# Optimization experiments

Hardware: AMD Instinct MI355X
Metric: run time of the kernel (lower is better)

Reference implementation:

```python
import jax, jax.numpy as jnp
import numpy as np

N_NODES = 100000
N_EDGES = 1600000
IN_DIM = 128
OUT_DIM = 128
NEG_SLOPE = 0.2


def setup_inputs() -> dict:
    key = jax.random.key(0)
    ks = jax.random.split(key, 7)
    x = jax.random.normal(ks[0], (N_NODES, IN_DIM), dtype=jnp.float32)
    edge_index = jax.random.randint(ks[1], (2, N_EDGES), 0, N_NODES, dtype=jnp.int32)
    # xavier-ish scale for [in, out] weight layout (y = x @ W)
    s = float(np.sqrt(2.0 / (IN_DIM + OUT_DIM)))
    W_q = jax.random.normal(ks[2], (IN_DIM, OUT_DIM), dtype=jnp.float32) * s
    W_k = jax.random.normal(ks[3], (IN_DIM, OUT_DIM), dtype=jnp.float32) * s
    W_v = jax.random.normal(ks[4], (IN_DIM, OUT_DIM), dtype=jnp.float32) * s
    W_l = jax.random.normal(ks[5], (IN_DIM, OUT_DIM), dtype=jnp.float32) * s
    b_l = jnp.zeros((OUT_DIM,), dtype=jnp.float32)
    return {"x": x, "edge_index": edge_index, "W_q": W_q, "W_k": W_k,
            "W_v": W_v, "W_l": W_l, "b_l": b_l}


def reference(x, edge_index, W_q, W_k, W_v, W_l, b_l):
    num_nodes = x.shape[0]
    row, col = edge_index[0], edge_index[1]

    h_q = x @ W_q                                   # [N, D]
    h_k = x @ W_k                                   # [N, D]
    _h_v = x @ W_v                                  # computed in original, unused downstream

    # aggregated query: sum of neighbor queries per destination node
    q_agg = jax.ops.segment_sum(h_q[col], row, num_segments=num_nodes)  # [N, D]
    k_act = jax.nn.leaky_relu(h_k, NEG_SLOPE)

    # per-edge attention scores (note: original uses raw q_agg, not activated)
    scores = jnp.sum(k_act[row] * q_agg[col], axis=1) / (OUT_DIM ** 0.5)  # [E]

    # scatter-softmax over edges grouped by destination (row)
    max_val = jax.ops.segment_max(scores, row, num_segments=num_nodes)
    exp_scores = jnp.exp(scores - max_val[row])
    sum_exp = jax.ops.segment_sum(exp_scores, row, num_segments=num_nodes)
    alpha = exp_scores / (sum_exp[row] + 1e-8)      # [E]; dropout is identity in eval

    h_proj = x @ W_l + b_l                          # [N, D]
    weighted = alpha[:, None] * h_proj[col]         # [E, D]
    h_prime = jax.ops.segment_sum(weighted, row, num_segments=num_nodes)
    return jax.nn.leaky_relu(h_prime, NEG_SLOPE)
```

## Files before the change

### kernel.cpp

```cpp
#include <hip/hip_runtime.h>
#include <math.h>

#define N_NODES 100000
#define N_EDGES 1600000
#define DIM 128
#define CAP 64

#define NB1 196
#define NPB 512
#define CHUNK1 4096
#define GRID1 391
#define SLOT1 52
#define LSTRIDE 197

typedef short bf16x8 __attribute__((ext_vector_type(8)));
typedef float f32x4 __attribute__((ext_vector_type(4)));

static __device__ __forceinline__ unsigned bf16rne(float f) {
    unsigned u = __float_as_uint(f);
    return (u + 0x7FFFu + ((u >> 16) & 1u)) >> 16;
}
static __device__ __forceinline__ float bflo(unsigned u) { return __uint_as_float(u << 16); }
static __device__ __forceinline__ float bfhi(unsigned u) { return __uint_as_float(u & 0xFFFF0000u); }


__global__ __launch_bounds__(256) void prep_k(
    const float* __restrict__ x, const float* __restrict__ Wq,
    const float* __restrict__ Wk, const float* __restrict__ Wl,
    ushort* __restrict__ xb, ushort* __restrict__ kactb,
    ushort* __restrict__ WqTh, ushort* __restrict__ WqTl,
    ushort* __restrict__ WlTh, ushort* __restrict__ WlTl) {
    __shared__ ushort bh[128 * 136];
    __shared__ ushort blo[128 * 136];
    int t = threadIdx.x;

    if (blockIdx.x < 2) {
        const float* W = (blockIdx.x == 0) ? Wq : Wl;
        ushort* Th = (blockIdx.x == 0) ? WqTh : WlTh;
        ushort* Tl = (blockIdx.x == 0) ? WqTl : WlTl;
        for (int i = t; i < 16384; i += 256) {
            int k = i >> 7, n = i & 127;
            float v = W[i];
            unsigned hi = bf16rne(v);
            float lo = v - bflo(hi);
            Th[n * 128 + k] = (ushort)hi;
            Tl[n * 128 + k] = (ushort)bf16rne(lo);
        }
    }
    for (int i = t; i < 16384; i += 256) {
        int k = i >> 7, n = i & 127;
        float v = Wk[i];
        unsigned hi = bf16rne(v);
        float lo = v - bflo(hi);
        bh[n * 136 + k] = (ushort)hi;
        blo[n * 136 + k] = (ushort)bf16rne(lo);
    }
    __syncthreads();

    int wave = t >> 6, lane = t & 63;
    int ln15 = lane & 15, quad = lane >> 4;
    long base = (long)blockIdx.x * 128 + wave * 32;

    bf16x8 Af[2][4];
#pragma unroll
    for (int r = 0; r < 2; r++) {
        long row = base + r * 16 + ln15;
        long rowc = row < N_NODES ? row : N_NODES - 1;
#pragma unroll
        for (int s = 0; s < 4; s++) {
            int ch = s * 4 + quad;
            const float4* xp = (const float4*)(x + rowc * 128 + ch * 8);
            float4 u0 = xp[0], u1 = xp[1];
            bf16x8 f;
            f[0] = (short)bf16rne(u0.x); f[1] = (short)bf16rne(u0.y);
            f[2] = (short)bf16rne(u0.z); f[3] = (short)bf16rne(u0.w);
            f[4] = (short)bf16rne(u1.x); f[5] = (short)bf16rne(u1.y);
            f[6] = (short)bf16rne(u1.z); f[7] = (short)bf16rne(u1.w);
            Af[r][s] = f;
            if (row < N_NODES) *(bf16x8*)(xb + row * 128 + ch * 8) = f;
        }
    }
    f32x4 acc[2][8];
#pragma unroll
    for (int r = 0; r < 2; r++)
#pragma unroll
        for (int t8 = 0; t8 < 8; t8++) acc[r][t8] = (f32x4){0.f, 0.f, 0.f, 0.f};
#pragma unroll
    for (int phase = 0; phase < 2; phase++) {
        const ushort* B = phase ? blo : bh;
#pragma unroll
        for (int s = 0; s < 4; s++) {
#pragma unroll
            for (int t8 = 0; t8 < 8; t8++) {
                bf16x8 b = *(const bf16x8*)(B + (t8 * 16 + ln15) * 136 + (s * 4 + quad) * 8);
                acc[0][t8] = __builtin_amdgcn_mfma_f32_16x16x32_bf16(Af[0][s], b, acc[0][t8], 0, 0, 0);
                acc[1][t8] = __builtin_amdgcn_mfma_f32_16x16x32_bf16(Af[1][s], b, acc[1][t8], 0, 0, 0);
            }
        }
    }
#pragma unroll
    for (int r = 0; r < 2; r++) {
#pragma unroll
        for (int reg = 0; reg < 4; reg++) {
            long node = base + r * 16 + quad * 4 + reg;
            if (node < N_NODES) {
#pragma unroll
                for (int t8 = 0; t8 < 8; t8++) {
                    float v = acc[r][t8][reg];
                    v = v > 0.f ? v : 0.2f * v;
                    kactb[node * 128 + t8 * 16 + ln15] = (ushort)bf16rne(v);
                }
            }
        }
    }
}


__global__ __launch_bounds__(256) void bin_k(const int* __restrict__ row,
                                             const int* __restrict__ col,
                                             unsigned* __restrict__ bkt,
                                             int* __restrict__ bktc) {
    __shared__ int lcnt[NB1];
    __shared__ unsigned lbuf[SLOT1 * LSTRIDE];
    int t = threadIdx.x, blk = blockIdx.x;
    if (t < NB1) lcnt[t] = 0;
    __syncthreads();
    long base = (long)blk * CHUNK1;
    if (base + CHUNK1 <= N_EDGES) {
        const uint4* r4 = (const uint4*)row + (size_t)blk * 1024;
        const uint4* c4 = (const uint4*)col + (size_t)blk * 1024;
#pragma unroll
        for (int q = 0; q < 4; q++) {
            uint4 rv = r4[q * 256 + t];
            uint4 cv = c4[q * 256 + t];
            unsigned rr[4] = {rv.x, rv.y, rv.z, rv.w};
            unsigned cc[4] = {cv.x, cv.y, cv.z, cv.w};
#pragma unroll
            for (int i = 0; i < 4; i++) {
                int b = rr[i] >> 9;
                int p = atomicAdd(&lcnt[b], 1);
                if (p < SLOT1) lbuf[p * LSTRIDE + b] = (cc[i] << 9) | (rr[i] & 511u);
            }
        }
    } else {
        for (int i = t; base + i < N_EDGES; i += 256) {
            unsigned r = (unsigned)row[base + i], c = (unsigned)col[base + i];
            int b = r >> 9;
            int p = atomicAdd(&lcnt[b], 1);
            if (p < SLOT1) lbuf[p * LSTRIDE + b] = (c << 9) | (r & 511u);
        }
    }
    __syncthreads();
    if (t < NB1) bktc[(size_t)blk * NB1 + t] = min(lcnt[t], SLOT1);
    int wave = t >> 6, lane = t & 63;
    for (int s = wave; s < NB1; s += 4) {
        if (lane < min(lcnt[s], SLOT1))
            bkt[((size_t)s * GRID1 + blk) * SLOT1 + lane] = lbuf[lane * LSTRIDE + s];
    }
}


__global__ __launch_bounds__(1024) void build_k(const int* __restrict__ bktc,
                                                const unsigned* __restrict__ bkt,
                                                int* __restrict__ cur,
                                                int* __restrict__ scol) {
    __shared__ int lcur[NPB];
    __shared__ int lc[GRID1];
    int b = blockIdx.x, t = threadIdx.x;
    if (t < NPB) lcur[t] = 0;
    if (t < GRID1) lc[t] = bktc[(size_t)t * NB1 + b];
    __syncthreads();
    int wave = t >> 6, lane = t & 63;
    const unsigned* D = bkt + (size_t)b * GRID1 * SLOT1;
    for (int s = wave; s < GRID1; s += 16) {
        if (lane < lc[s]) {
            unsigned v = D[(size_t)s * SLOT1 + lane];
            int rl = (int)(v & 511u);
            int c = (int)(v >> 9);
            int p = atomicAdd(&lcur[rl], 1);
            if (p < CAP) scol[((size_t)b * NPB + rl) * CAP + p] = c;
        }
    }
    __syncthreads();
    if (t < NPB) {
        int node = b * NPB + t;
        if (node < N_NODES) cur[node] = lcur[t];
    }
}


__global__ __launch_bounds__(1024) void xq_k(const uint4* __restrict__ xb4,
                                             const int* __restrict__ cur,
                                             const int* __restrict__ scol,
                                             const ushort* __restrict__ BTh,
                                             const ushort* __restrict__ BTl,
                                             uint4* __restrict__ qx4) {
    __shared__ ushort lxa[64][136];
    __shared__ ushort lq[64][136];
    int t = threadIdx.x;
    int g16 = t >> 4, gl = t & 15;
    long node = (long)blockIdx.x * 64 + g16;
    int d = (node < N_NODES) ? min(cur[node], CAP) : 0;
    float a0 = 0.f, a1 = 0.f, a2 = 0.f, a3 = 0.f;
    float a4 = 0.f, a5 = 0.f, a6 = 0.f, a7 = 0.f;
    for (int j = 0; j < d; j += 16) {
        int cb = (j + gl < d) ? scol[node * CAP + j + gl] : 0;
        int lim = min(16, d - j);
        int k = 0;
        for (; k + 4 <= lim; k += 4) {
            int c0 = __shfl(cb, k, 16),     c1 = __shfl(cb, k + 1, 16);
            int c2 = __shfl(cb, k + 2, 16), c3 = __shfl(cb, k + 3, 16);
            uint4 u0 = xb4[(size_t)c0 * 16 + gl];
            uint4 u1 = xb4[(size_t)c1 * 16 + gl];
            uint4 u2 = xb4[(size_t)c2 * 16 + gl];
            uint4 u3 = xb4[(size_t)c3 * 16 + gl];
            a0 += bflo(u0.x); a1 += bfhi(u0.x); a2 += bflo(u0.y); a3 += bfhi(u0.y);
            a4 += bflo(u0.z); a5 += bfhi(u0.z); a6 += bflo(u0.w); a7 += bfhi(u0.w);
            a0 += bflo(u1.x); a1 += bfhi(u1.x); a2 += bflo(u1.y); a3 += bfhi(u1.y);
            a4 += bflo(u1.z); a5 += bfhi(u1.z); a6 += bflo(u1.w); a7 += bfhi(u1.w);
            a0 += bflo(u2.x); a1 += bfhi(u2.x); a2 += bflo(u2.y); a3 += bfhi(u2.y);
            a4 += bflo(u2.z); a5 += bfhi(u2.z); a6 += bflo(u2.w); a7 += bfhi(u2.w);
            a0 += bflo(u3.x); a1 += bfhi(u3.x); a2 += bflo(u3.y); a3 += bfhi(u3.y);
            a4 += bflo(u3.z); a5 += bfhi(u3.z); a6 += bflo(u3.w); a7 += bfhi(u3.w);
        }
        for (; k < lim; k++) {
            int c = __shfl(cb, k, 16);
            uint4 u = xb4[(size_t)c * 16 + gl];
            a0 += bflo(u.x); a1 += bfhi(u.x); a2 += bflo(u.y); a3 += bfhi(u.y);
            a4 += bflo(u.z); a5 += bfhi(u.z); a6 += bflo(u.w); a7 += bfhi(u.w);
        }
    }
    uint4 o;
    o.x = bf16rne(a0) | (bf16rne(a1) << 16);
    o.y = bf16rne(a2) | (bf16rne(a3) << 16);
    o.z = bf16rne(a4) | (bf16rne(a5) << 16);
    o.w = bf16rne(a6) | (bf16rne(a7) << 16);
    *(uint4*)&lxa[g16][gl * 8] = o;
    __syncthreads();

    int wave = t >> 6, lane = t & 63;
    int ln15 = lane & 15, quad = (lane >> 4) & 3;
    const bf16x8* Bh8 = (const bf16x8*)BTh;
    const bf16x8* Bl8 = (const bf16x8*)BTl;
#pragma unroll
    for (int ti = 0; ti < 2; ti++) {
        int T = wave + ti * 16;
        int rt = T & 3, ct = T >> 2;
        bf16x8 af[4];
#pragma unroll
        for (int s = 0; s < 4; s++)
            af[s] = *(const bf16x8*)&lxa[rt * 16 + ln15][(s * 4 + quad) * 8];
        f32x4 acc = (f32x4){0.f, 0.f, 0.f, 0.f};
#pragma unroll
        for (int phase = 0; phase < 2; phase++) {
            const bf16x8* B8 = phase ? Bl8 : Bh8;
#pragma unroll
            for (int s = 0; s < 4; s++)
                acc = __builtin_amdgcn_mfma_f32_16x16x32_bf16(
                    af[s], B8[(ct * 16 + ln15) * 16 + s * 4 + quad], acc, 0, 0, 0);
        }
#pragma unroll
        for (int reg = 0; reg < 4; reg++)
            lq[rt * 16 + quad * 4 + reg][ct * 16 + ln15] = (ushort)bf16rne(acc[reg]);
    }
    __syncthreads();

    const uint2* xb2 = (const uint2*)xb4;
#pragma unroll
    for (int i = 0; i < 2; i++) {
        int idx = i * 1024 + t;
        int g = idx >> 5, c = idx & 31;
        long n2 = (long)blockIdx.x * 64 + g;
        if (n2 < N_NODES) {
            uint2 q2 = *(const uint2*)&lq[g][c * 4];
            uint2 x2 = xb2[n2 * 32 + c];
            qx4[n2 * 32 + c] = make_uint4(q2.x, q2.y, x2.x, x2.y);
        }
    }
}


__global__ __launch_bounds__(256) void attn_k(const uint2* __restrict__ kactb,
                                              const uint4* __restrict__ qx4,
                                              const int* __restrict__ cur,
                                              const int* __restrict__ scol,
                                              uint2* __restrict__ xwb,
                                              float* __restrict__ sumw) {
    int g = (blockIdx.x * 256 + threadIdx.x) >> 5;
    int lane = threadIdx.x & 31;
    int d = min(cur[g], CAP);
    uint2 ku = kactb[(size_t)g * 32 + lane];
    const float scale = 0.08838834764831845f;
    float k0 = bflo(ku.x) * scale, k1 = bfhi(ku.x) * scale;
    float k2 = bflo(ku.y) * scale, k3 = bfhi(ku.y) * scale;

    float S = 0.f;
    float a0 = 0.f, a1 = 0.f, a2 = 0.f, a3 = 0.f;
    for (int j = 0; j < d; j += 32) {
        int cb = (j + lane < d) ? scol[g * CAP + j + lane] : 0;
        int lim = min(32, d - j);
        int k = 0;
        for (; k + 4 <= lim; k += 4) {
            int c0 = __shfl(cb, k, 32),     c1 = __shfl(cb, k + 1, 32);
            int c2 = __shfl(cb, k + 2, 32), c3 = __shfl(cb, k + 3, 32);
            uint4 u0 = qx4[(size_t)c0 * 32 + lane];
            uint4 u1 = qx4[(size_t)c1 * 32 + lane];
            uint4 u2 = qx4[(size_t)c2 * 32 + lane];
            uint4 u3 = qx4[(size_t)c3 * 32 + lane];
            float p0 = k0 * bflo(u0.x) + k1 * bfhi(u0.x) + k2 * bflo(u0.y) + k3 * bfhi(u0.y);
            float p1 = k0 * bflo(u1.x) + k1 * bfhi(u1.x) + k2 * bflo(u1.y) + k3 * bfhi(u1.y);
            float p2 = k0 * bflo(u2.x) + k1 * bfhi(u2.x) + k2 * bflo(u2.y) + k3 * bfhi(u2.y);
            float p3 = k0 * bflo(u3.x) + k1 * bfhi(u3.x) + k2 * bflo(u3.y) + k3 * bfhi(u3.y);
#pragma unroll
            for (int off = 16; off > 0; off >>= 1) {
                p0 += __shfl_xor(p0, off, 32); p1 += __shfl_xor(p1, off, 32);
                p2 += __shfl_xor(p2, off, 32); p3 += __shfl_xor(p3, off, 32);
            }
            float e0 = __expf(p0), e1 = __expf(p1);
            float e2 = __expf(p2), e3 = __expf(p3);
            S += (e0 + e1) + (e2 + e3);
            a0 += e0 * bflo(u0.z) + e1 * bflo(u1.z) + e2 * bflo(u2.z) + e3 * bflo(u3.z);
            a1 += e0 * bfhi(u0.z) + e1 * bfhi(u1.z) + e2 * bfhi(u2.z) + e3 * bfhi(u3.z);
            a2 += e0 * bflo(u0.w) + e1 * bflo(u1.w) + e2 * bflo(u2.w) + e3 * bflo(u3.w);
            a3 += e0 * bfhi(u0.w) + e1 * bfhi(u1.w) + e2 * bfhi(u2.w) + e3 * bfhi(u3.w);
        }
        for (; k < lim; k++) {
            int c = __shfl(cb, k, 32);
            uint4 u = qx4[(size_t)c * 32 + lane];
            float p = k0 * bflo(u.x) + k1 * bfhi(u.x) + k2 * bflo(u.y) + k3 * bfhi(u.y);
#pragma unroll
            for (int off = 16; off > 0; off >>= 1) p += __shfl_xor(p, off, 32);
            float e0 = __expf(p);
            S += e0;
            a0 += e0 * bflo(u.z);
            a1 += e0 * bfhi(u.z);
            a2 += e0 * bflo(u.w);
            a3 += e0 * bfhi(u.w);
        }
    }
    float inv = 1.f / (S + 1e-8f);
    uint2 o;
    o.x = bf16rne(a0 * inv) | (bf16rne(a1 * inv) << 16);
    o.y = bf16rne(a2 * inv) | (bf16rne(a3 * inv) << 16);
    xwb[(size_t)g * 32 + lane] = o;
    if (lane == 0) sumw[g] = S * inv;
}


__global__ __launch_bounds__(256) void fin_k(const ushort* __restrict__ Ab,
                                             const ushort* __restrict__ BTh,
                                             const ushort* __restrict__ BTl,
                                             const float* __restrict__ bl,
                                             const float* __restrict__ sumw,
                                             float* __restrict__ out) {
    int tid = threadIdx.x;
    int wave = tid >> 6, lane = tid & 63;
    int ln15 = lane & 15, quad = (lane >> 4) & 3;
    long base = (long)blockIdx.x * 128 + wave * 32;

    const bf16x8* A8 = (const bf16x8*)Ab;
    const bf16x8* Bh8 = (const bf16x8*)BTh;
    const bf16x8* Bl8 = (const bf16x8*)BTl;

    bf16x8 Af[2][4];
#pragma unroll
    for (int r = 0; r < 2; r++) {
        long row = base + r * 16 + ln15;
#pragma unroll
        for (int s = 0; s < 4; s++) Af[r][s] = A8[row * 16 + s * 4 + quad];
    }
    float blv[8];
#pragma unroll
    for (int t = 0; t < 8; t++) blv[t] = bl[t * 16 + ln15];

    f32x4 acc[2][8];
#pragma unroll
    for (int r = 0; r < 2; r++)
#pragma unroll
        for (int t = 0; t < 8; t++) acc[r][t] = (f32x4){0.f, 0.f, 0.f, 0.f};

#pragma unroll
    for (int phase = 0; phase < 2; phase++) {
        const bf16x8* B8 = phase ? Bl8 : Bh8;
#pragma unroll
        for (int s = 0; s < 4; s++) {
#pragma unroll
            for (int t = 0; t < 8; t++) {
                bf16x8 b = B8[(t * 16 + ln15) * 16 + s * 4 + quad];
                acc[0][t] = __builtin_amdgcn_mfma_f32_16x16x32_bf16(Af[0][s], b, acc[0][t], 0, 0, 0);
                acc[1][t] = __builtin_amdgcn_mfma_f32_16x16x32_bf16(Af[1][s], b, acc[1][t], 0, 0, 0);
            }
        }
    }
#pragma unroll
    for (int r = 0; r < 2; r++) {
#pragma unroll
        for (int reg = 0; reg < 4; reg++) {
            long node = base + r * 16 + quad * 4 + reg;
            if (node < N_NODES) {
                float sw = sumw[node];
#pragma unroll
                for (int t = 0; t < 8; t++) {
                    float v = acc[r][t][reg] + sw * blv[t];
                    v = v > 0.f ? v : 0.2f * v;
                    out[node * 128 + t * 16 + ln15] = v;
                }
            }
        }
    }
}


extern "C" void kernel_launch(void* const* d_in, const int* in_sizes, int n_in,
                              void* d_out, int out_size, void* d_ws, size_t ws_size,
                              hipStream_t stream) {
    const float* x  = (const float*)d_in[0];
    const int* row  = (const int*)d_in[1];
    const int* col  = row + N_EDGES;
    const float* Wq = (const float*)d_in[2];
    const float* Wk = (const float*)d_in[3];
    const float* Wl = (const float*)d_in[5];
    const float* bl = (const float*)d_in[6];
    float* out = (float*)d_out;

    ushort* xb    = (ushort*)d_ws;
    ushort* qx    = xb + (size_t)N_NODES * DIM;
    ushort* kactb = qx + (size_t)N_NODES * 256;
    ushort* xwb   = kactb + (size_t)N_NODES * DIM;
    ushort* wbuf  = xwb + (size_t)N_NODES * DIM;
    ushort* WqTh = wbuf,             *WqTl = wbuf + 16384;
    ushort* WlTh = wbuf + 2 * 16384, *WlTl = wbuf + 3 * 16384;
    float* sumw = (float*)(wbuf + 4 * 16384);
    int* cur  = (int*)(sumw + N_NODES);
    int* scol = cur + N_NODES;
    unsigned* bkt = (unsigned*)(scol + (size_t)N_NODES * CAP);
    int* bktc = (int*)(bkt + (size_t)NB1 * GRID1 * SLOT1);

    prep_k<<<782, 256, 0, stream>>>(x, Wq, Wk, Wl, xb, kactb,
                                    WqTh, WqTl, WlTh, WlTl);
    bin_k<<<GRID1, 256, 0, stream>>>(row, col, bkt, bktc);
    build_k<<<NB1, 1024, 0, stream>>>(bktc, bkt, cur, scol);
    xq_k<<<(N_NODES + 63) / 64, 1024, 0, stream>>>((const uint4*)xb, cur, scol,
                                                   WqTh, WqTl, (uint4*)qx);
    attn_k<<<N_NODES / 8, 256, 0, stream>>>((const uint2*)kactb, (const uint4*)qx,
                                            cur, scol, (uint2*)xwb, sumw);
    fin_k<<<(N_NODES + 127) / 128, 256, 0, stream>>>(xwb, WlTh, WlTl, bl, sumw, out);
}
```

Before: 490.0 us.

## Fuse edge binning into prep kernel and shrink xq_k blocks to 16 nodes

Merges the bin_k edge-bucketing kernel into the prep kernel. Every third block does binning and the others do the x conversion and K projection, so the two independent phases run concurrently and one launch is removed. Separately, xq_k is reshaped from 1024-thread blocks covering 64 nodes to 256-thread blocks covering 16 nodes. This uses less LDS per block and loads the A fragment once per wave, but each block now reads the Wq fragments from global memory with less reuse. The shared smem buffer is sized for the larger of the two roles, which may limit occupancy for the binning blocks.

Result: faster. 458.5 us (-6.4%).

```diff
diff --git a/kernel.cpp b/kernel.cpp
--- a/kernel.cpp
+++ b/kernel.cpp
@@ -24,20 +24,66 @@
 static __device__ __forceinline__ float bfhi(unsigned u) { return __uint_as_float(u & 0xFFFF0000u); }
 
 
-__global__ __launch_bounds__(256) void prep_k(
+__global__ __launch_bounds__(256) void pb_k(
     const float* __restrict__ x, const float* __restrict__ Wq,
     const float* __restrict__ Wk, const float* __restrict__ Wl,
+    const int* __restrict__ row, const int* __restrict__ col,
     ushort* __restrict__ xb, ushort* __restrict__ kactb,
     ushort* __restrict__ WqTh, ushort* __restrict__ WqTl,
-    ushort* __restrict__ WlTh, ushort* __restrict__ WlTl) {
-    __shared__ ushort bh[128 * 136];
-    __shared__ ushort blo[128 * 136];
-    int t = threadIdx.x;
-
-    if (blockIdx.x < 2) {
-        const float* W = (blockIdx.x == 0) ? Wq : Wl;
-        ushort* Th = (blockIdx.x == 0) ? WqTh : WlTh;
-        ushort* Tl = (blockIdx.x == 0) ? WqTl : WlTl;
+    ushort* __restrict__ WlTh, ushort* __restrict__ WlTl,
+    unsigned* __restrict__ bkt, int* __restrict__ bktc) {
+    __shared__ uint4 smem4[4352];
+    int j = blockIdx.x, t = threadIdx.x;
+
+    if (j % 3 == 2) {
+        int blk = j / 3;
+        int* lcnt = (int*)smem4;
+        unsigned* lbuf = (unsigned*)smem4 + 256;
+        if (t < NB1) lcnt[t] = 0;
+        __syncthreads();
+        long base = (long)blk * CHUNK1;
+        if (base + CHUNK1 <= N_EDGES) {
+            const uint4* r4 = (const uint4*)row + (size_t)blk * 1024;
+            const uint4* c4 = (const uint4*)col + (size_t)blk * 1024;
+#pragma unroll
+            for (int q = 0; q < 4; q++) {
+                uint4 rv = r4[q * 256 + t];
+                uint4 cv = c4[q * 256 + t];
+                unsigned rr[4] = {rv.x, rv.y, rv.z, rv.w};
+                unsigned cc[4] = {cv.x, cv.y, cv.z, cv.w};
+#pragma unroll
+                for (int i = 0; i < 4; i++) {
+                    int b = rr[i] >> 9;
+                    int p = atomicAdd(&lcnt[b], 1);
+                    if (p < SLOT1) lbuf[p * LSTRIDE + b] = (cc[i] << 9) | (rr[i] & 511u);
+                }
+            }
+        } else {
+            for (int i = t; base + i < N_EDGES; i += 256) {
+                unsigned r = (unsigned)row[base + i], c = (unsigned)col[base + i];
+                int b = r >> 9;
+                int p = atomicAdd(&lcnt[b], 1);
+                if (p < SLOT1) lbuf[p * LSTRIDE + b] = (c << 9) | (r & 511u);
+            }
+        }
+        __syncthreads();
+        if (t < NB1) bktc[(size_t)blk * NB1 + t] = min(lcnt[t], SLOT1);
+        int wave = t >> 6, lane = t & 63;
+        for (int s = wave; s < NB1; s += 4) {
+            if (lane < min(lcnt[s], SLOT1))
+                bkt[((size_t)s * GRID1 + blk) * SLOT1 + lane] = lbuf[lane * LSTRIDE + s];
+        }
+        return;
+    }
+
+    int p = (j / 3) * 2 + (j % 3);
+    ushort* bh = (ushort*)smem4;
+    ushort* blo = (ushort*)smem4 + 128 * 136;
+
+    if (p < 2) {
+        const float* W = (p == 0) ? Wq : Wl;
+        ushort* Th = (p == 0) ? WqTh : WlTh;
+        ushort* Tl = (p == 0) ? WqTl : WlTl;
         for (int i = t; i < 16384; i += 256) {
             int k = i >> 7, n = i & 127;
             float v = W[i];
@@ -59,13 +105,13 @@
 
     int wave = t >> 6, lane = t & 63;
     int ln15 = lane & 15, quad = lane >> 4;
-    long base = (long)blockIdx.x * 128 + wave * 32;
+    long base = (long)p * 128 + wave * 32;
 
     bf16x8 Af[2][4];
 #pragma unroll
     for (int r = 0; r < 2; r++) {
-        long row = base + r * 16 + ln15;
-        long rowc = row < N_NODES ? row : N_NODES - 1;
+        long rw = base + r * 16 + ln15;
+        long rowc = rw < N_NODES ? rw : N_NODES - 1;
 #pragma unroll
         for (int s = 0; s < 4; s++) {
             int ch = s * 4 + quad;
@@ -77,7 +123,7 @@
             f[4] = (short)bf16rne(u1.x); f[5] = (short)bf16rne(u1.y);
             f[6] = (short)bf16rne(u1.z); f[7] = (short)bf16rne(u1.w);
             Af[r][s] = f;
-            if (row < N_NODES) *(bf16x8*)(xb + row * 128 + ch * 8) = f;
+            if (rw < N_NODES) *(bf16x8*)(xb + rw * 128 + ch * 8) = f;
         }
     }
     f32x4 acc[2][8];
@@ -112,50 +158,6 @@
                 }
             }
         }
-    }
-}
-
-
-__global__ __launch_bounds__(256) void bin_k(const int* __restrict__ row,
-                                             const int* __restrict__ col,
-                                             unsigned* __restrict__ bkt,
-                                             int* __restrict__ bktc) {
-    __shared__ int lcnt[NB1];
-    __shared__ unsigned lbuf[SLOT1 * LSTRIDE];
-    int t = threadIdx.x, blk = blockIdx.x;
-    if (t < NB1) lcnt[t] = 0;
-    __syncthreads();
-    long base = (long)blk * CHUNK1;
-    if (base + CHUNK1 <= N_EDGES) {
-        const uint4* r4 = (const uint4*)row + (size_t)blk * 1024;
-        const uint4* c4 = (const uint4*)col + (size_t)blk * 1024;
-#pragma unroll
-        for (int q = 0; q < 4; q++) {
-            uint4 rv = r4[q * 256 + t];
-            uint4 cv = c4[q * 256 + t];
-            unsigned rr[4] = {rv.x, rv.y, rv.z, rv.w};
-            unsigned cc[4] = {cv.x, cv.y, cv.z, cv.w};
-#pragma unroll
-            for (int i = 0; i < 4; i++) {
-                int b = rr[i] >> 9;
-                int p = atomicAdd(&lcnt[b], 1);
-                if (p < SLOT1) lbuf[p * LSTRIDE + b] = (cc[i] << 9) | (rr[i] & 511u);
-            }
-        }
-    } else {
-        for (int i = t; base + i < N_EDGES; i += 256) {
-            unsigned r = (unsigned)row[base + i], c = (unsigned)col[base + i];
-            int b = r >> 9;
-            int p = atomicAdd(&lcnt[b], 1);
-            if (p < SLOT1) lbuf[p * LSTRIDE + b] = (c << 9) | (r & 511u);
-        }
-    }
-    __syncthreads();
-    if (t < NB1) bktc[(size_t)blk * NB1 + t] = min(lcnt[t], SLOT1);
-    int wave = t >> 6, lane = t & 63;
-    for (int s = wave; s < NB1; s += 4) {
-        if (lane < min(lcnt[s], SLOT1))
-            bkt[((size_t)s * GRID1 + blk) * SLOT1 + lane] = lbuf[lane * LSTRIDE + s];
     }
 }
 
@@ -189,18 +191,18 @@
 }
 
 
-__global__ __launch_bounds__(1024) void xq_k(const uint4* __restrict__ xb4,
-                                             const int* __restrict__ cur,
-                                             const int* __restrict__ scol,
-                                             const ushort* __restrict__ BTh,
-                                             const ushort* __restrict__ BTl,
-                                             uint4* __restrict__ qx4) {
-    __shared__ ushort lxa[64][136];
-    __shared__ ushort lq[64][136];
+__global__ __launch_bounds__(256) void xq_k(const uint4* __restrict__ xb4,
+                                            const int* __restrict__ cur,
+                                            const int* __restrict__ scol,
+                                            const ushort* __restrict__ BTh,
+                                            const ushort* __restrict__ BTl,
+                                            uint4* __restrict__ qx4) {
+    __shared__ ushort lxa[16][136];
+    __shared__ ushort lq[16][136];
     int t = threadIdx.x;
     int g16 = t >> 4, gl = t & 15;
-    long node = (long)blockIdx.x * 64 + g16;
-    int d = (node < N_NODES) ? min(cur[node], CAP) : 0;
+    long node = (long)blockIdx.x * 16 + g16;
+    int d = min(cur[node], CAP);
     float a0 = 0.f, a1 = 0.f, a2 = 0.f, a3 = 0.f;
     float a4 = 0.f, a5 = 0.f, a6 = 0.f, a7 = 0.f;
     for (int j = 0; j < d; j += 16) {
@@ -242,14 +244,13 @@
     int ln15 = lane & 15, quad = (lane >> 4) & 3;
     const bf16x8* Bh8 = (const bf16x8*)BTh;
     const bf16x8* Bl8 = (const bf16x8*)BTl;
+    bf16x8 af[4];
+#pragma unroll
+    for (int s = 0; s < 4; s++)
+        af[s] = *(const bf16x8*)&lxa[ln15][(s * 4 + quad) * 8];
 #pragma unroll
     for (int ti = 0; ti < 2; ti++) {
-        int T = wave + ti * 16;
-        int rt = T & 3, ct = T >> 2;
-        bf16x8 af[4];
-#pragma unroll
-        for (int s = 0; s < 4; s++)
-            af[s] = *(const bf16x8*)&lxa[rt * 16 + ln15][(s * 4 + quad) * 8];
+        int ct = wave * 2 + ti;
         f32x4 acc = (f32x4){0.f, 0.f, 0.f, 0.f};
 #pragma unroll
         for (int phase = 0; phase < 2; phase++) {
@@ -261,21 +262,19 @@
         }
 #pragma unroll
         for (int reg = 0; reg < 4; reg++)
-            lq[rt * 16 + quad * 4 + reg][ct * 16 + ln15] = (ushort)bf16rne(acc[reg]);
+            lq[quad * 4 + reg][ct * 16 + ln15] = (ushort)bf16rne(acc[reg]);
     }
     __syncthreads();
 
     const uint2* xb2 = (const uint2*)xb4;
 #pragma unroll
     for (int i = 0; i < 2; i++) {
-        int idx = i * 1024 + t;
+        int idx = i * 256 + t;
         int g = idx >> 5, c = idx & 31;
-        long n2 = (long)blockIdx.x * 64 + g;
-        if (n2 < N_NODES) {
-            uint2 q2 = *(const uint2*)&lq[g][c * 4];
-            uint2 x2 = xb2[n2 * 32 + c];
-            qx4[n2 * 32 + c] = make_uint4(q2.x, q2.y, x2.x, x2.y);
-        }
+        long n2 = (long)blockIdx.x * 16 + g;
+        uint2 q2 = *(const uint2*)&lq[g][c * 4];
+        uint2 x2 = xb2[n2 * 32 + c];
+        qx4[n2 * 32 + c] = make_uint4(q2.x, q2.y, x2.x, x2.y);
     }
 }
 
@@ -436,12 +435,11 @@
     unsigned* bkt = (unsigned*)(scol + (size_t)N_NODES * CAP);
     int* bktc = (int*)(bkt + (size_t)NB1 * GRID1 * SLOT1);
 
-    prep_k<<<782, 256, 0, stream>>>(x, Wq, Wk, Wl, xb, kactb,
-                                    WqTh, WqTl, WlTh, WlTl);
-    bin_k<<<GRID1, 256, 0, stream>>>(row, col, bkt, bktc);
+    pb_k<<<1173, 256, 0, stream>>>(x, Wq, Wk, Wl, row, col, xb, kactb,
+                                   WqTh, WqTl, WlTh, WlTl, bkt, bktc);
     build_k<<<NB1, 1024, 0, stream>>>(bktc, bkt, cur, scol);
-    xq_k<<<(N_NODES + 63) / 64, 1024, 0, stream>>>((const uint4*)xb, cur, scol,
-                                                   WqTh, WqTl, (uint4*)qx);
+    xq_k<<<N_NODES / 16, 256, 0, stream>>>((const uint4*)xb, cur, scol,
+                                           WqTh, WqTl, (uint4*)qx);
     attn_k<<<N_NODES / 8, 256, 0, stream>>>((const uint2*)kactb, (const uint4*)qx,
                                             cur, scol, (uint2*)xwb, sumw);
     fin_k<<<(N_NODES + 127) / 128, 256, 0, stream>>>(xwb, WlTh, WlTl, bl, sumw, out);
```
